# Performance work log

Hardware: AMD Instinct MI355X
Metric: run time of the kernel (lower is better)

The kernel has to match this reference:

```python
import jax, jax.numpy as jnp
import numpy as np

N_HEADS = 16
CONTEXT_WINDOW = 256


def _band_mask(s_q, s_k):
    # True = masked out. Module (causal=True, context_window=256) allows only
    # keys with 0 <= (query_pos - key_pos) < CONTEXT_WINDOW (causal mask is
    # subsumed by the lower band).
    d = jnp.arange(s_q)[:, None] - jnp.arange(s_k)[None, :]
    return ~((d >= 0) & (d < CONTEXT_WINDOW))


def setup_inputs() -> dict:
    key = jax.random.key(0)
    ks = jax.random.split(key, 5)
    B, S, D = 2, 2048, 1024
    std = 0.02
    return {
        "query": jax.random.normal(ks[0], (B, S, D), dtype=jnp.float32),
        "Wq": jax.random.normal(ks[1], (D, D), dtype=jnp.float32) * std,
        "bq": jnp.zeros((D,), dtype=jnp.float32),
        "Wk": jax.random.normal(ks[2], (D, D), dtype=jnp.float32) * std,
        "bk": jnp.zeros((D,), dtype=jnp.float32),
        "Wv": jax.random.normal(ks[3], (D, D), dtype=jnp.float32) * std,
        "bv": jnp.zeros((D,), dtype=jnp.float32),
        "Wo": jax.random.normal(ks[4], (D, D), dtype=jnp.float32) * std,
        "bo": jnp.zeros((D,), dtype=jnp.float32),
    }


def reference(query, Wq, bq, Wk, bk, Wv, bv, Wo, bo):
    B, S, D = query.shape
    H = N_HEADS
    Dh = D // H
    # projections -> [B, H, S, Dh]
    q = (query @ Wq + bq).reshape(B, S, H, Dh).transpose(0, 2, 1, 3)
    k = (query @ Wk + bk).reshape(B, S, H, Dh).transpose(0, 2, 1, 3)
    v = (query @ Wv + bv).reshape(B, S, H, Dh).transpose(0, 2, 1, 3)
    scores = jnp.einsum("bhqd,bhkd->bhqk", q, k) * (1.0 / np.sqrt(Dh))
    mask = _band_mask(S, S)  # [S, S]
    scores = jnp.where(mask[None, None, :, :], -jnp.inf, scores)
    attn = jax.nn.softmax(scores, axis=-1)
    out = jnp.einsum("bhqk,bhkd->bhqd", attn, v)
    out = out.transpose(0, 2, 1, 3).reshape(B, S, D)
    return out @ Wo + bo
```

## Files before the change

### kernel.cpp

```cpp
#include <hip/hip_runtime.h>
#include <hip/hip_bf16.h>


typedef __bf16 bf16x8 __attribute__((ext_vector_type(8)));
typedef float f32x4 __attribute__((ext_vector_type(4)));
typedef short s16x4 __attribute__((ext_vector_type(4)));
typedef unsigned short u16x8 __attribute__((ext_vector_type(8)));
typedef unsigned short u16x4 __attribute__((ext_vector_type(4)));

__device__ __forceinline__ unsigned short f2bf(float f) {
  unsigned int u = __builtin_bit_cast(unsigned int, f);
  u += 0x7FFFu + ((u >> 16) & 1u);
  return (unsigned short)(u >> 16);
}

__device__ __forceinline__ f32x4 mfma32(bf16x8 a, bf16x8 b, f32x4 c) {
  return __builtin_amdgcn_mfma_f32_16x16x32_bf16(a, b, c, 0, 0, 0);
}
__device__ __forceinline__ f32x4 mfma16(s16x4 a, s16x4 b, f32x4 c) {
  return __builtin_amdgcn_mfma_f32_16x16x16bf16_1k(a, b, c, 0, 0, 0);
}

__device__ __forceinline__ void gl16(const unsigned short* gsrc,
                                     unsigned short* lds) {
  __builtin_amdgcn_global_load_lds(
      (const __attribute__((address_space(1))) unsigned int*)gsrc,
      (__attribute__((address_space(3))) unsigned int*)lds, 16, 0, 0);
}

__global__ __launch_bounds__(256) void cvt_all(
    const float* __restrict__ x,
    const float* __restrict__ Wq, const float* __restrict__ Wk,
    const float* __restrict__ Wv, const float* __restrict__ Wo,
    unsigned short* __restrict__ xb, unsigned short* __restrict__ Wt) {
  const int z = blockIdx.z;
  const int tx = threadIdx.x, ty = threadIdx.y;
  if (z == 4) {
    const int tid = (blockIdx.y * 32 + blockIdx.x) * 256 + ty * 32 + tx;
#pragma unroll
    for (int it = 0; it < 4; ++it) {
      const int i = tid + it * 262144;
      const float4 v = ((const float4*)x)[i];
      u16x4 o = { f2bf(v.x), f2bf(v.y), f2bf(v.z), f2bf(v.w) };
      *(u16x4*)(xb + (size_t)i * 4) = o;
    }
    return;
  }
  const float* W = (z == 0) ? Wq : (z == 1) ? Wk : (z == 2) ? Wv : Wo;
  unsigned short* dst = Wt + (size_t)z * 1024 * 1024;
  __shared__ float t[32][33];
  const int n0 = blockIdx.x * 32, k0 = blockIdx.y * 32;
#pragma unroll
  for (int i = 0; i < 32; i += 8)
    t[ty + i][tx] = W[(size_t)(k0 + ty + i) * 1024 + n0 + tx];
  __syncthreads();
#pragma unroll
  for (int i = 0; i < 32; i += 8)
    dst[(size_t)(n0 + ty + i) * 1024 + k0 + tx] = f2bf(t[tx][ty + i]);
}

template <int BN, int MODE>
__global__ __launch_bounds__(256) void gemm_lds(
    const unsigned short* __restrict__ A, const unsigned short* __restrict__ Bt,
    const float* __restrict__ bq, const float* __restrict__ bk,
    const float* __restrict__ bv,
    unsigned short* __restrict__ q_ws, unsigned short* __restrict__ k_ws,
    unsigned short* __restrict__ v_ws,
    const float* __restrict__ bo, float* __restrict__ outp) {
  constexpr int ACC_N = BN / 32;
  __shared__ unsigned short Alds[128 * 32];
  __shared__ unsigned short Blds[BN * 32];
  const int tid = threadIdx.x, lane = tid & 63, w = tid >> 6;
  const int lq = lane & 15, lg = lane >> 4;
  const int bm = blockIdx.x, bn = blockIdx.y;
  const int wr = (w >> 1) * 64, wc = (w & 1) * (BN / 2);

  const int srow = lane >> 2, scol8 = (lane & 3) * 8;
  const unsigned short* Ag =
      A + (size_t)(bm * 128 + w * 32 + srow) * 1024 + scol8;
  const unsigned short* Bg =
      (BN == 128) ? Bt + (size_t)(bn * 128 + w * 32 + srow) * 1024 + scol8
                  : Bt + (size_t)(bn * 64 + w * 16 + srow) * 1024 + scol8;
  unsigned short* Al0 = Alds + (w * 32) * 32;
  unsigned short* Al1 = Alds + (w * 32 + 16) * 32;
  unsigned short* Bl0 = (BN == 128) ? Blds + (w * 32) * 32
                                    : Blds + (w * 16) * 32;
  unsigned short* Bl1 = Blds + (w * 32 + 16) * 32;

  f32x4 acc[4][ACC_N] = {};
  for (int kt = 0; kt < 1024; kt += 32) {
    __syncthreads();
    gl16(Ag + kt, Al0);
    gl16(Ag + kt + 16 * 1024, Al1);
    gl16(Bg + kt, Bl0);
    if (BN == 128) gl16(Bg + kt + 16 * 1024, Bl1);
    __syncthreads();
    bf16x8 af[4], bfr[ACC_N];
#pragma unroll
    for (int m = 0; m < 4; ++m)
      af[m] = *(const bf16x8*)(Alds + (wr + m * 16 + lq) * 32 + lg * 8);
#pragma unroll
    for (int n = 0; n < ACC_N; ++n)
      bfr[n] = *(const bf16x8*)(Blds + (wc + n * 16 + lq) * 32 + lg * 8);
#pragma unroll
    for (int m = 0; m < 4; ++m)
#pragma unroll
      for (int n = 0; n < ACC_N; ++n)
        acc[m][n] = mfma32(af[m], bfr[n], acc[m][n]);
  }

  const int r0 = bm * 128 + wr + lg * 4;
  const int c0g = bn * BN + wc + lq;
#pragma unroll
  for (int m = 0; m < 4; ++m) {
#pragma unroll
    for (int n = 0; n < ACC_N; ++n) {
      const int col = c0g + n * 16;
#pragma unroll
      for (int j = 0; j < 4; ++j) {
        const int row = r0 + m * 16 + j;
        float v = acc[m][n][j];
        if (MODE == 0) {
          const int t = col >> 10, cc = col & 1023;
          const float* bias = (t == 0) ? bq : ((t == 1) ? bk : bv);
          v += bias[cc];
          if (t == 0) v *= 0.125f;
          unsigned short* dst = (t == 0) ? q_ws : ((t == 1) ? k_ws : v_ws);
          const int h = cc >> 6, dh = cc & 63, b = row >> 11, s = row & 2047;
          dst[((size_t)(b * 16 + h) * 2048 + s) * 64 + dh] = f2bf(v);
        } else {
          outp[(size_t)row * 1024 + col] = v + bo[col];
        }
      }
    }
  }
}

__global__ __launch_bounds__(256) void attn_kernel(
    const unsigned short* __restrict__ q_ws,
    const unsigned short* __restrict__ k_ws,
    const unsigned short* __restrict__ v_ws,
    unsigned short* __restrict__ attn_out) {
  __shared__ unsigned short o_lds[4][16 * 64];
  const int tid = threadIdx.x, lane = tid & 63, w = tid >> 6;
  const int lq = lane & 15, lg = lane >> 4;
  const int bh = blockIdx.y;
  const int q0 = blockIdx.x * 64 + w * 16;
  const unsigned short* Q = q_ws + (size_t)bh * 2048 * 64;
  const unsigned short* Kp = k_ws + (size_t)bh * 2048 * 64;
  const unsigned short* Vp = v_ws + (size_t)bh * 2048 * 64;

  const bf16x8 qf0 = *(const bf16x8*)(Q + (size_t)(q0 + lq) * 64 + lg * 8);
  const bf16x8 qf1 = *(const bf16x8*)(Q + (size_t)(q0 + lq) * 64 + 32 + lg * 8);

  float lsum = 0.f;
  f32x4 oacc[4] = {};
  int t0 = (q0 - 255) >> 4;
  if (t0 < 0) t0 = 0;
  const int t1 = q0 >> 4;

  for (int t = t0; t <= t1; ++t) {
    const int j0 = t * 16;
    const bf16x8 kf0 = *(const bf16x8*)(Kp + (size_t)(j0 + lq) * 64 + lg * 8);
    const bf16x8 kf1 =
        *(const bf16x8*)(Kp + (size_t)(j0 + lq) * 64 + 32 + lg * 8);
    f32x4 st = {};
    st = mfma32(kf0, qf0, st);
    st = mfma32(kf1, qf1, st);

    float p[4], ps = 0.f;
#pragma unroll
    for (int r = 0; r < 4; ++r) {
      const int delta = (q0 + lq) - (j0 + lg * 4 + r);
      const bool ok = (delta >= 0) && (delta < 256);
      p[r] = ok ? __expf(st[r] - 4.0f) : 0.f;
      ps += p[r];
    }
    ps += __shfl_xor(ps, 16);
    ps += __shfl_xor(ps, 32);
    lsum += ps;

    s16x4 pb = { (short)f2bf(p[0]), (short)f2bf(p[1]),
                 (short)f2bf(p[2]), (short)f2bf(p[3]) };
#pragma unroll
    for (int c = 0; c < 4; ++c) {
      s16x4 vf;
#pragma unroll
      for (int j = 0; j < 4; ++j)
        vf[j] = (short)Vp[(size_t)(j0 + lg * 4 + j) * 64 + c * 16 + lq];
      oacc[c] = mfma16(vf, pb, oacc[c]);
    }
  }

  const float rl = 1.f / lsum;
#pragma unroll
  for (int c = 0; c < 4; ++c)
#pragma unroll
    for (int r = 0; r < 4; ++r)
      o_lds[w][lq * 64 + c * 16 + lg * 4 + r] = f2bf(oacc[c][r] * rl);
  __syncthreads();
  const int row = lane >> 2, d0 = (lane & 3) * 16;
  const u16x8 o0 = *(const u16x8*)(&o_lds[w][row * 64 + d0]);
  const u16x8 o1 = *(const u16x8*)(&o_lds[w][row * 64 + d0 + 8]);
  const size_t g =
      ((size_t)((bh >> 4) * 2048 + q0 + row)) * 1024 + (bh & 15) * 64 + d0;
  *(u16x8*)(attn_out + g) = o0;
  *(u16x8*)(attn_out + g + 8) = o1;
}

extern "C" void kernel_launch(void* const* d_in, const int* in_sizes, int n_in,
                              void* d_out, int out_size, void* d_ws,
                              size_t ws_size, hipStream_t stream) {
  const float* query = (const float*)d_in[0];
  const float* Wq = (const float*)d_in[1];
  const float* bq = (const float*)d_in[2];
  const float* Wk = (const float*)d_in[3];
  const float* bk = (const float*)d_in[4];
  const float* Wv = (const float*)d_in[5];
  const float* bv = (const float*)d_in[6];
  const float* Wo = (const float*)d_in[7];
  const float* bo = (const float*)d_in[8];
  float* outp = (float*)d_out;

  char* ws = (char*)d_ws;
  unsigned short* xbf = (unsigned short*)(ws);
  unsigned short* wt  = (unsigned short*)(ws + (8u << 20));
  unsigned short* qws = (unsigned short*)(ws + (16u << 20));
  unsigned short* kws = (unsigned short*)(ws + (24u << 20));
  unsigned short* vws = (unsigned short*)(ws + (32u << 20));

  cvt_all<<<dim3(32, 32, 5), dim3(32, 8), 0, stream>>>(query, Wq, Wk, Wv, Wo,
                                                       xbf, wt);
  gemm_lds<128, 0><<<dim3(32, 24), 256, 0, stream>>>(
      xbf, wt, bq, bk, bv, qws, kws, vws, nullptr, nullptr);
  attn_kernel<<<dim3(32, 32), 256, 0, stream>>>(qws, kws, vws, xbf);
  gemm_lds<64, 1><<<dim3(32, 16), 256, 0, stream>>>(
      xbf, wt + (size_t)3 * 1024 * 1024, nullptr, nullptr, nullptr, nullptr,
      nullptr, nullptr, bo, outp);
}
```

Before: 93.29 us.

## Rewrite QKV projection GEMM with 256x256 tiles and triple-buffered LDS pipeline

Replaces the templated QKV GEMM with a dedicated 512-thread kernel that computes 256x256 output tiles. It stages A and B into LDS through a three-slot ring with manual vmcnt waits, so global loads for step t+2 overlap the MFMAs of step t. It also XOR-swizzles the LDS columns to avoid bank conflicts and raises wave priority around the MFMA blocks. The grid shrinks to 192 blocks, which may underfill the GPU's compute units, and the larger register and LDS footprint limits occupancy.

New measurement: 103.3 us. 10.7% more time.

```diff
diff --git a/kernel.cpp b/kernel.cpp
--- a/kernel.cpp
+++ b/kernel.cpp
@@ -59,81 +59,169 @@
     dst[(size_t)(n0 + ty + i) * 1024 + k0 + tx] = f2bf(t[tx][ty + i]);
 }
 
-template <int BN, int MODE>
-__global__ __launch_bounds__(256) void gemm_lds(
+__global__ __launch_bounds__(512, 2) void gemm_qkv(
     const unsigned short* __restrict__ A, const unsigned short* __restrict__ Bt,
     const float* __restrict__ bq, const float* __restrict__ bk,
     const float* __restrict__ bv,
     unsigned short* __restrict__ q_ws, unsigned short* __restrict__ k_ws,
-    unsigned short* __restrict__ v_ws,
-    const float* __restrict__ bo, float* __restrict__ outp) {
-  constexpr int ACC_N = BN / 32;
-  __shared__ unsigned short Alds[128 * 32];
-  __shared__ unsigned short Blds[BN * 32];
+    unsigned short* __restrict__ v_ws) {
+  __shared__ __align__(16) unsigned short Alds[3][8192];
+  __shared__ __align__(16) unsigned short Blds[3][8192];
   const int tid = threadIdx.x, lane = tid & 63, w = tid >> 6;
   const int lq = lane & 15, lg = lane >> 4;
   const int bm = blockIdx.x, bn = blockIdx.y;
-  const int wr = (w >> 1) * 64, wc = (w & 1) * (BN / 2);
+  const int wr = (w >> 2) * 128, wc = (w & 3) * 64;
+
+  const int srow = tid >> 2;
+  const int scs = ((tid & 3) ^ ((tid >> 3) & 3)) << 3;
+  const unsigned short* Ag = A + (size_t)(bm * 256 + srow) * 1024 + scs;
+  const unsigned short* Bg = Bt + (size_t)(bn * 256 + srow) * 1024 + scs;
+
+  auto stageA = [&](int kt2, int s2, int i) {
+    gl16(Ag + (size_t)i * 128 * 1024 + kt2, &Alds[s2][i * 4096 + w * 512]);
+  };
+  auto stageB = [&](int kt2, int s2, int i) {
+    gl16(Bg + (size_t)i * 128 * 1024 + kt2, &Blds[s2][i * 4096 + w * 512]);
+  };
+
+  const int cs = (lq >> 1) & 3;
+  auto rdA = [&](int s, int m) {
+    return *(const bf16x8*)(&Alds[s][(wr + m * 16 + lq) * 32 +
+                                     ((lg ^ cs) << 3)]);
+  };
+  auto rdB = [&](int s, int n) {
+    return *(const bf16x8*)(&Blds[s][(wc + n * 16 + lq) * 32 +
+                                     ((lg ^ cs) << 3)]);
+  };
+
+  f32x4 acc[8][4] = {};
+  stageA(0, 0, 0); stageA(0, 0, 1); stageB(0, 0, 0); stageB(0, 0, 1);
+  stageA(32, 1, 0); stageA(32, 1, 1); stageB(32, 1, 0); stageB(32, 1, 1);
+
+  int s = 0;
+  for (int t = 0; t < 32; ++t) {
+    if (t < 31) asm volatile("s_waitcnt vmcnt(4)" ::: "memory");
+    else        asm volatile("s_waitcnt vmcnt(0)" ::: "memory");
+    asm volatile("s_barrier" ::: "memory");
+    const int kt2 = (t + 2) * 32;
+    const int s2 = (s == 0) ? 2 : s - 1;
+    const bool st = (t < 30);
+    bf16x8 am[4], bf[4];
+    if (st) stageA(kt2, s2, 0);
+#pragma unroll
+    for (int m = 0; m < 4; ++m) am[m] = rdA(s, m);
+    bf[0] = rdB(s, 0); bf[1] = rdB(s, 1);
+    __builtin_amdgcn_s_setprio(1);
+#pragma unroll
+    for (int m = 0; m < 4; ++m) {
+      acc[m][0] = mfma32(am[m], bf[0], acc[m][0]);
+      acc[m][1] = mfma32(am[m], bf[1], acc[m][1]);
+    }
+    __builtin_amdgcn_s_setprio(0);
+    if (st) stageA(kt2, s2, 1);
+    bf[2] = rdB(s, 2); bf[3] = rdB(s, 3);
+    __builtin_amdgcn_s_setprio(1);
+#pragma unroll
+    for (int m = 0; m < 4; ++m) {
+      acc[m][2] = mfma32(am[m], bf[2], acc[m][2]);
+      acc[m][3] = mfma32(am[m], bf[3], acc[m][3]);
+    }
+    __builtin_amdgcn_s_setprio(0);
+    if (st) stageB(kt2, s2, 0);
+#pragma unroll
+    for (int m = 0; m < 4; ++m) am[m] = rdA(s, m + 4);
+    __builtin_amdgcn_s_setprio(1);
+#pragma unroll
+    for (int m = 0; m < 4; ++m) {
+      acc[m + 4][0] = mfma32(am[m], bf[0], acc[m + 4][0]);
+      acc[m + 4][1] = mfma32(am[m], bf[1], acc[m + 4][1]);
+    }
+    __builtin_amdgcn_s_setprio(0);
+    if (st) stageB(kt2, s2, 1);
+    __builtin_amdgcn_s_setprio(1);
+#pragma unroll
+    for (int m = 0; m < 4; ++m) {
+      acc[m + 4][2] = mfma32(am[m], bf[2], acc[m + 4][2]);
+      acc[m + 4][3] = mfma32(am[m], bf[3], acc[m + 4][3]);
+    }
+    __builtin_amdgcn_s_setprio(0);
+    s = (s == 2) ? 0 : s + 1;
+  }
+
+  const int ttype = bn >> 2;
+  const float* bias = (ttype == 0) ? bq : (ttype == 1) ? bk : bv;
+  unsigned short* dst = (ttype == 0) ? q_ws : (ttype == 1) ? k_ws : v_ws;
+  const float scalef = (ttype == 0) ? 0.125f : 1.0f;
+  const int ccb = (bn & 3) * 256 + wc + lq;
+  const int r0 = bm * 256 + wr + lg * 4;
+#pragma unroll
+  for (int m = 0; m < 8; ++m) {
+#pragma unroll
+    for (int n = 0; n < 4; ++n) {
+      const int cc = ccb + n * 16;
+      const int h = cc >> 6, dh = cc & 63;
+#pragma unroll
+      for (int j = 0; j < 4; ++j) {
+        const int row = r0 + m * 16 + j;
+        const int b = row >> 11, sq = row & 2047;
+        const float v = (acc[m][n][j] + bias[cc]) * scalef;
+        dst[((size_t)(b * 16 + h) * 2048 + sq) * 64 + dh] = f2bf(v);
+      }
+    }
+  }
+}
+
+__global__ __launch_bounds__(256) void gemm_out(
+    const unsigned short* __restrict__ A, const unsigned short* __restrict__ Bt,
+    const float* __restrict__ bo, float* __restrict__ outp) {
+  __shared__ unsigned short Alds[128 * 32];
+  __shared__ unsigned short Blds[64 * 32];
+  const int tid = threadIdx.x, lane = tid & 63, w = tid >> 6;
+  const int lq = lane & 15, lg = lane >> 4;
+  const int bm = blockIdx.x, bn = blockIdx.y;
+  const int wr = (w >> 1) * 64, wc = (w & 1) * 32;
 
   const int srow = lane >> 2, scol8 = (lane & 3) * 8;
   const unsigned short* Ag =
       A + (size_t)(bm * 128 + w * 32 + srow) * 1024 + scol8;
   const unsigned short* Bg =
-      (BN == 128) ? Bt + (size_t)(bn * 128 + w * 32 + srow) * 1024 + scol8
-                  : Bt + (size_t)(bn * 64 + w * 16 + srow) * 1024 + scol8;
+      Bt + (size_t)(bn * 64 + w * 16 + srow) * 1024 + scol8;
   unsigned short* Al0 = Alds + (w * 32) * 32;
   unsigned short* Al1 = Alds + (w * 32 + 16) * 32;
-  unsigned short* Bl0 = (BN == 128) ? Blds + (w * 32) * 32
-                                    : Blds + (w * 16) * 32;
-  unsigned short* Bl1 = Blds + (w * 32 + 16) * 32;
-
-  f32x4 acc[4][ACC_N] = {};
+  unsigned short* Bl0 = Blds + (w * 16) * 32;
+
+  f32x4 acc[4][2] = {};
   for (int kt = 0; kt < 1024; kt += 32) {
     __syncthreads();
     gl16(Ag + kt, Al0);
     gl16(Ag + kt + 16 * 1024, Al1);
     gl16(Bg + kt, Bl0);
-    if (BN == 128) gl16(Bg + kt + 16 * 1024, Bl1);
     __syncthreads();
-    bf16x8 af[4], bfr[ACC_N];
+    bf16x8 af[4], bfr[2];
 #pragma unroll
     for (int m = 0; m < 4; ++m)
       af[m] = *(const bf16x8*)(Alds + (wr + m * 16 + lq) * 32 + lg * 8);
 #pragma unroll
-    for (int n = 0; n < ACC_N; ++n)
+    for (int n = 0; n < 2; ++n)
       bfr[n] = *(const bf16x8*)(Blds + (wc + n * 16 + lq) * 32 + lg * 8);
 #pragma unroll
     for (int m = 0; m < 4; ++m)
 #pragma unroll
-      for (int n = 0; n < ACC_N; ++n)
+      for (int n = 0; n < 2; ++n)
         acc[m][n] = mfma32(af[m], bfr[n], acc[m][n]);
   }
 
   const int r0 = bm * 128 + wr + lg * 4;
-  const int c0g = bn * BN + wc + lq;
-#pragma unroll
-  for (int m = 0; m < 4; ++m) {
-#pragma unroll
-    for (int n = 0; n < ACC_N; ++n) {
+  const int c0g = bn * 64 + wc + lq;
+#pragma unroll
+  for (int m = 0; m < 4; ++m)
+#pragma unroll
+    for (int n = 0; n < 2; ++n) {
       const int col = c0g + n * 16;
 #pragma unroll
-      for (int j = 0; j < 4; ++j) {
-        const int row = r0 + m * 16 + j;
-        float v = acc[m][n][j];
-        if (MODE == 0) {
-          const int t = col >> 10, cc = col & 1023;
-          const float* bias = (t == 0) ? bq : ((t == 1) ? bk : bv);
-          v += bias[cc];
-          if (t == 0) v *= 0.125f;
-          unsigned short* dst = (t == 0) ? q_ws : ((t == 1) ? k_ws : v_ws);
-          const int h = cc >> 6, dh = cc & 63, b = row >> 11, s = row & 2047;
-          dst[((size_t)(b * 16 + h) * 2048 + s) * 64 + dh] = f2bf(v);
-        } else {
-          outp[(size_t)row * 1024 + col] = v + bo[col];
-        }
-      }
-    }
-  }
+      for (int j = 0; j < 4; ++j)
+        outp[(size_t)(r0 + m * 16 + j) * 1024 + col] = acc[m][n][j] + bo[col];
+    }
 }
 
 __global__ __launch_bounds__(256) void attn_kernel(
@@ -164,16 +252,16 @@
     const bf16x8 kf0 = *(const bf16x8*)(Kp + (size_t)(j0 + lq) * 64 + lg * 8);
     const bf16x8 kf1 =
         *(const bf16x8*)(Kp + (size_t)(j0 + lq) * 64 + 32 + lg * 8);
-    f32x4 st = {};
-    st = mfma32(kf0, qf0, st);
-    st = mfma32(kf1, qf1, st);
+    f32x4 stv = {};
+    stv = mfma32(kf0, qf0, stv);
+    stv = mfma32(kf1, qf1, stv);
 
     float p[4], ps = 0.f;
 #pragma unroll
     for (int r = 0; r < 4; ++r) {
       const int delta = (q0 + lq) - (j0 + lg * 4 + r);
       const bool ok = (delta >= 0) && (delta < 256);
-      p[r] = ok ? __expf(st[r] - 4.0f) : 0.f;
+      p[r] = ok ? __expf(stv[r] - 4.0f) : 0.f;
       ps += p[r];
     }
     ps += __shfl_xor(ps, 16);
@@ -231,10 +319,9 @@
 
   cvt_all<<<dim3(32, 32, 5), dim3(32, 8), 0, stream>>>(query, Wq, Wk, Wv, Wo,
                                                        xbf, wt);
-  gemm_lds<128, 0><<<dim3(32, 24), 256, 0, stream>>>(
-      xbf, wt, bq, bk, bv, qws, kws, vws, nullptr, nullptr);
+  gemm_qkv<<<dim3(16, 12), 512, 0, stream>>>(xbf, wt, bq, bk, bv, qws, kws,
+                                             vws);
   attn_kernel<<<dim3(32, 32), 256, 0, stream>>>(qws, kws, vws, xbf);
-  gemm_lds<64, 1><<<dim3(32, 16), 256, 0, stream>>>(
-      xbf, wt + (size_t)3 * 1024 * 1024, nullptr, nullptr, nullptr, nullptr,
-      nullptr, nullptr, bo, outp);
-}
+  gemm_out<<<dim3(32, 16), 256, 0, stream>>>(
+      xbf, wt + (size_t)3 * 1024 * 1024, bo, outp);
+}
```

## Double GEMM K-tile to 64 with XOR-swizzled LDS layout

Applied to the files above, without the earlier changes.

The LDS-staged GEMM now loads a 64-wide K slab per iteration instead of 32. This halves the number of __syncthreads barrier pairs and global-to-LDS rounds. The LDS layout uses an XOR swizzle of the 8-element column chunks by row to avoid bank conflicts on the fragment reads. LDS use doubles, which may reduce occupancy, and the attention kernel only gets a variable rename.

New measurement: 95.92 us. +2.8%, slower.

```diff
diff --git a/kernel.cpp b/kernel.cpp
--- a/kernel.cpp
+++ b/kernel.cpp
@@ -68,45 +68,52 @@
     unsigned short* __restrict__ v_ws,
     const float* __restrict__ bo, float* __restrict__ outp) {
   constexpr int ACC_N = BN / 32;
-  __shared__ unsigned short Alds[128 * 32];
-  __shared__ unsigned short Blds[BN * 32];
+  constexpr int BI = BN / 32;
+  __shared__ __align__(16) unsigned short Alds[128 * 64];
+  __shared__ __align__(16) unsigned short Blds[BN * 64];
   const int tid = threadIdx.x, lane = tid & 63, w = tid >> 6;
   const int lq = lane & 15, lg = lane >> 4;
   const int bm = blockIdx.x, bn = blockIdx.y;
   const int wr = (w >> 1) * 64, wc = (w & 1) * (BN / 2);
 
-  const int srow = lane >> 2, scol8 = (lane & 3) * 8;
+  const int lrow = lane >> 3;
+  const int ksw = (((lane & 7) ^ lrow) << 3);
   const unsigned short* Ag =
-      A + (size_t)(bm * 128 + w * 32 + srow) * 1024 + scol8;
+      A + (size_t)(bm * 128 + w * 32 + lrow) * 1024 + ksw;
   const unsigned short* Bg =
-      (BN == 128) ? Bt + (size_t)(bn * 128 + w * 32 + srow) * 1024 + scol8
-                  : Bt + (size_t)(bn * 64 + w * 16 + srow) * 1024 + scol8;
-  unsigned short* Al0 = Alds + (w * 32) * 32;
-  unsigned short* Al1 = Alds + (w * 32 + 16) * 32;
-  unsigned short* Bl0 = (BN == 128) ? Blds + (w * 32) * 32
-                                    : Blds + (w * 16) * 32;
-  unsigned short* Bl1 = Blds + (w * 32 + 16) * 32;
+      Bt + (size_t)(bn * BN + w * (BN / 4) + lrow) * 1024 + ksw;
+  unsigned short* AlW = Alds + (w * 32) * 64;
+  unsigned short* BlW = Blds + (w * (BN / 4)) * 64;
+
+  const int cs = lq & 7;
 
   f32x4 acc[4][ACC_N] = {};
-  for (int kt = 0; kt < 1024; kt += 32) {
+  for (int kt = 0; kt < 1024; kt += 64) {
     __syncthreads();
-    gl16(Ag + kt, Al0);
-    gl16(Ag + kt + 16 * 1024, Al1);
-    gl16(Bg + kt, Bl0);
-    if (BN == 128) gl16(Bg + kt + 16 * 1024, Bl1);
+#pragma unroll
+    for (int i = 0; i < 4; ++i)
+      gl16(Ag + kt + (size_t)i * 8 * 1024, AlW + i * 8 * 64);
+#pragma unroll
+    for (int i = 0; i < BI; ++i)
+      gl16(Bg + kt + (size_t)i * 8 * 1024, BlW + i * 8 * 64);
     __syncthreads();
-    bf16x8 af[4], bfr[ACC_N];
-#pragma unroll
-    for (int m = 0; m < 4; ++m)
-      af[m] = *(const bf16x8*)(Alds + (wr + m * 16 + lq) * 32 + lg * 8);
-#pragma unroll
-    for (int n = 0; n < ACC_N; ++n)
-      bfr[n] = *(const bf16x8*)(Blds + (wc + n * 16 + lq) * 32 + lg * 8);
-#pragma unroll
-    for (int m = 0; m < 4; ++m)
+#pragma unroll
+    for (int kk = 0; kk < 2; ++kk) {
+      bf16x8 af[4], bfr[ACC_N];
+#pragma unroll
+      for (int m = 0; m < 4; ++m)
+        af[m] = *(const bf16x8*)(Alds + (wr + m * 16 + lq) * 64 +
+                                 (((kk * 4 + lg) ^ cs) << 3));
 #pragma unroll
       for (int n = 0; n < ACC_N; ++n)
-        acc[m][n] = mfma32(af[m], bfr[n], acc[m][n]);
+        bfr[n] = *(const bf16x8*)(Blds + (wc + n * 16 + lq) * 64 +
+                                  (((kk * 4 + lg) ^ cs) << 3));
+#pragma unroll
+      for (int m = 0; m < 4; ++m)
+#pragma unroll
+        for (int n = 0; n < ACC_N; ++n)
+          acc[m][n] = mfma32(af[m], bfr[n], acc[m][n]);
+    }
   }
 
   const int r0 = bm * 128 + wr + lg * 4;
@@ -164,16 +171,16 @@
     const bf16x8 kf0 = *(const bf16x8*)(Kp + (size_t)(j0 + lq) * 64 + lg * 8);
     const bf16x8 kf1 =
         *(const bf16x8*)(Kp + (size_t)(j0 + lq) * 64 + 32 + lg * 8);
-    f32x4 st = {};
-    st = mfma32(kf0, qf0, st);
-    st = mfma32(kf1, qf1, st);
+    f32x4 stv = {};
+    stv = mfma32(kf0, qf0, stv);
+    stv = mfma32(kf1, qf1, stv);
 
     float p[4], ps = 0.f;
 #pragma unroll
     for (int r = 0; r < 4; ++r) {
       const int delta = (q0 + lq) - (j0 + lg * 4 + r);
       const bool ok = (delta >= 0) && (delta < 256);
-      p[r] = ok ? __expf(st[r] - 4.0f) : 0.f;
+      p[r] = ok ? __expf(stv[r] - 4.0f) : 0.f;
       ps += p[r];
     }
     ps += __shfl_xor(ps, 16);
```

## Stage GEMM epilogues through swizzled LDS and store V transposed for attention

Applied to the files above, without the earlier changes.

Both GEMM epilogues now stage accumulators through an XOR-swizzled shared-memory tile in two passes, then write to global memory with 16-byte vector stores instead of scattered scalar stores. The QKV GEMM writes V in a transposed [bh][dh][s] layout with a padded row stride. The attention kernel can then load V fragments as single contiguous 4-element vectors rather than four strided scalar loads. The cost is extra LDS round trips and barriers in the epilogue, plus a gather-style LDS read when transposing V.

After: 126.5 us. 1.36x slower.

```diff
diff --git a/kernel.cpp b/kernel.cpp
--- a/kernel.cpp
+++ b/kernel.cpp
@@ -65,11 +65,12 @@
     const float* __restrict__ bq, const float* __restrict__ bk,
     const float* __restrict__ bv,
     unsigned short* __restrict__ q_ws, unsigned short* __restrict__ k_ws,
-    unsigned short* __restrict__ v_ws,
+    unsigned short* __restrict__ vt_ws,
     const float* __restrict__ bo, float* __restrict__ outp) {
   constexpr int ACC_N = BN / 32;
-  __shared__ unsigned short Alds[128 * 32];
-  __shared__ unsigned short Blds[BN * 32];
+  __shared__ __align__(16) unsigned short smem[8192];
+  unsigned short* Alds = smem;
+  unsigned short* Blds = smem + 4096;
   const int tid = threadIdx.x, lane = tid & 63, w = tid >> 6;
   const int lq = lane & 15, lg = lane >> 4;
   const int bm = blockIdx.x, bn = blockIdx.y;
@@ -109,28 +110,89 @@
         acc[m][n] = mfma32(af[m], bfr[n], acc[m][n]);
   }
 
-  const int r0 = bm * 128 + wr + lg * 4;
-  const int c0g = bn * BN + wc + lq;
-#pragma unroll
-  for (int m = 0; m < 4; ++m) {
-#pragma unroll
-    for (int n = 0; n < ACC_N; ++n) {
-      const int col = c0g + n * 16;
-#pragma unroll
-      for (int j = 0; j < 4; ++j) {
-        const int row = r0 + m * 16 + j;
-        float v = acc[m][n][j];
-        if (MODE == 0) {
-          const int t = col >> 10, cc = col & 1023;
-          const float* bias = (t == 0) ? bq : ((t == 1) ? bk : bv);
-          v += bias[cc];
-          if (t == 0) v *= 0.125f;
-          unsigned short* dst = (t == 0) ? q_ws : ((t == 1) ? k_ws : v_ws);
-          const int h = cc >> 6, dh = cc & 63, b = row >> 11, s = row & 2047;
-          dst[((size_t)(b * 16 + h) * 2048 + s) * 64 + dh] = f2bf(v);
-        } else {
-          outp[(size_t)row * 1024 + col] = v + bo[col];
+  if (MODE == 0) {
+    const int ttype = bn >> 3;
+    const float* bias = (ttype == 0) ? bq : (ttype == 1) ? bk : bv;
+    const float scalef = (ttype == 0) ? 0.125f : 1.0f;
+#pragma unroll
+    for (int p = 0; p < 2; ++p) {
+      __syncthreads();
+      if ((w >> 1) == p) {
+#pragma unroll
+        for (int m = 0; m < 4; ++m)
+#pragma unroll
+          for (int n = 0; n < 4; ++n)
+#pragma unroll
+            for (int j = 0; j < 4; ++j) {
+              const int lrow = m * 16 + lg * 4 + j;
+              const int col = wc + n * 16 + lq;
+              const float v =
+                  (acc[m][n][j] + bias[(bn & 7) * 128 + col]) * scalef;
+              smem[lrow * 128 + (((col >> 3) ^ (lrow & 15)) << 3) +
+                   (col & 7)] = f2bf(v);
+            }
+      }
+      __syncthreads();
+      const int grow = bm * 128 + p * 64;
+      const int b = grow >> 11;
+      if (ttype < 2) {
+        const int lr = tid & 63, seg = tid >> 6;
+        const int s = (grow & 2047) + lr;
+        const int h = (bn & 7) * 2 + (seg >> 1), dh0 = (seg & 1) * 32;
+        unsigned short* dst = ((ttype == 0) ? q_ws : k_ws) +
+                              ((size_t)(b * 16 + h) * 2048 + s) * 64 + dh0;
+#pragma unroll
+        for (int j2 = 0; j2 < 4; ++j2) {
+          const int c = seg * 4 + j2;
+          *(u16x8*)(dst + j2 * 8) =
+              *(const u16x8*)&smem[lr * 128 + ((c ^ (lr & 15)) << 3)];
         }
+      } else {
+        const int pair = tid >> 1, sh = tid & 1;
+        const int h = (bn & 7) * 2 + (pair >> 6), dh = pair & 63;
+        const int s0 = (grow & 2047) + sh * 32;
+        unsigned short* dst =
+            vt_ws + ((size_t)(b * 16 + h) * 64 + dh) * 2080 + s0;
+#pragma unroll
+        for (int i = 0; i < 4; ++i) {
+          u16x8 val;
+#pragma unroll
+          for (int e = 0; e < 8; ++e) {
+            const int lr = sh * 32 + i * 8 + e;
+            val[e] = smem[lr * 128 + (((pair >> 3) ^ (lr & 15)) << 3) +
+                          (pair & 7)];
+          }
+          *(u16x8*)(dst + i * 8) = val;
+        }
+      }
+    }
+  } else {
+    float* Cf = (float*)smem;
+#pragma unroll
+    for (int p = 0; p < 2; ++p) {
+      __syncthreads();
+      if ((w >> 1) == p) {
+#pragma unroll
+        for (int m = 0; m < 4; ++m)
+#pragma unroll
+          for (int n = 0; n < 2; ++n)
+#pragma unroll
+            for (int j = 0; j < 4; ++j) {
+              const int lrow = m * 16 + lg * 4 + j;
+              const int col = wc + n * 16 + lq;
+              Cf[lrow * 64 + (((col >> 2) ^ (lrow & 15)) << 2) + (col & 3)] =
+                  acc[m][n][j] + bo[bn * 64 + col];
+            }
+      }
+      __syncthreads();
+      const int row = tid >> 2, seg = tid & 3;
+      float* dst = outp + (size_t)(bm * 128 + p * 64 + row) * 1024 +
+                   bn * 64 + seg * 16;
+#pragma unroll
+      for (int j2 = 0; j2 < 4; ++j2) {
+        const int c = seg * 4 + j2;
+        ((float4*)dst)[j2] =
+            *(const float4*)&Cf[row * 64 + ((c ^ (row & 15)) << 2)];
       }
     }
   }
@@ -139,7 +201,7 @@
 __global__ __launch_bounds__(256) void attn_kernel(
     const unsigned short* __restrict__ q_ws,
     const unsigned short* __restrict__ k_ws,
-    const unsigned short* __restrict__ v_ws,
+    const unsigned short* __restrict__ vt_ws,
     unsigned short* __restrict__ attn_out) {
   __shared__ unsigned short o_lds[4][16 * 64];
   const int tid = threadIdx.x, lane = tid & 63, w = tid >> 6;
@@ -148,7 +210,7 @@
   const int q0 = blockIdx.x * 64 + w * 16;
   const unsigned short* Q = q_ws + (size_t)bh * 2048 * 64;
   const unsigned short* Kp = k_ws + (size_t)bh * 2048 * 64;
-  const unsigned short* Vp = v_ws + (size_t)bh * 2048 * 64;
+  const unsigned short* Vt = vt_ws + (size_t)bh * 64 * 2080;
 
   const bf16x8 qf0 = *(const bf16x8*)(Q + (size_t)(q0 + lq) * 64 + lg * 8);
   const bf16x8 qf1 = *(const bf16x8*)(Q + (size_t)(q0 + lq) * 64 + 32 + lg * 8);
@@ -164,16 +226,16 @@
     const bf16x8 kf0 = *(const bf16x8*)(Kp + (size_t)(j0 + lq) * 64 + lg * 8);
     const bf16x8 kf1 =
         *(const bf16x8*)(Kp + (size_t)(j0 + lq) * 64 + 32 + lg * 8);
-    f32x4 st = {};
-    st = mfma32(kf0, qf0, st);
-    st = mfma32(kf1, qf1, st);
+    f32x4 stv = {};
+    stv = mfma32(kf0, qf0, stv);
+    stv = mfma32(kf1, qf1, stv);
 
     float p[4], ps = 0.f;
 #pragma unroll
     for (int r = 0; r < 4; ++r) {
       const int delta = (q0 + lq) - (j0 + lg * 4 + r);
       const bool ok = (delta >= 0) && (delta < 256);
-      p[r] = ok ? __expf(st[r] - 4.0f) : 0.f;
+      p[r] = ok ? __expf(stv[r] - 4.0f) : 0.f;
       ps += p[r];
     }
     ps += __shfl_xor(ps, 16);
@@ -184,10 +246,8 @@
                  (short)f2bf(p[2]), (short)f2bf(p[3]) };
 #pragma unroll
     for (int c = 0; c < 4; ++c) {
-      s16x4 vf;
-#pragma unroll
-      for (int j = 0; j < 4; ++j)
-        vf[j] = (short)Vp[(size_t)(j0 + lg * 4 + j) * 64 + c * 16 + lq];
+      const s16x4 vf =
+          *(const s16x4*)(Vt + (size_t)(c * 16 + lq) * 2080 + j0 + lg * 4);
       oacc[c] = mfma16(vf, pb, oacc[c]);
     }
   }
@@ -227,13 +287,13 @@
   unsigned short* wt  = (unsigned short*)(ws + (8u << 20));
   unsigned short* qws = (unsigned short*)(ws + (16u << 20));
   unsigned short* kws = (unsigned short*)(ws + (24u << 20));
-  unsigned short* vws = (unsigned short*)(ws + (32u << 20));
+  unsigned short* vtw = (unsigned short*)(ws + (32u << 20));
 
   cvt_all<<<dim3(32, 32, 5), dim3(32, 8), 0, stream>>>(query, Wq, Wk, Wv, Wo,
                                                        xbf, wt);
   gemm_lds<128, 0><<<dim3(32, 24), 256, 0, stream>>>(
-      xbf, wt, bq, bk, bv, qws, kws, vws, nullptr, nullptr);
-  attn_kernel<<<dim3(32, 32), 256, 0, stream>>>(qws, kws, vws, xbf);
+      xbf, wt, bq, bk, bv, qws, kws, vtw, nullptr, nullptr);
+  attn_kernel<<<dim3(32, 32), 256, 0, stream>>>(qws, kws, vtw, xbf);
   gemm_lds<64, 1><<<dim3(32, 16), 256, 0, stream>>>(
       xbf, wt + (size_t)3 * 1024 * 1024, nullptr, nullptr, nullptr, nullptr,
       nullptr, nullptr, bo, outp);
```
